# Optimization experiments

Measured on AMD Instinct MI355X. Metric: run time of the kernel, lower is better.

## Reference

```python
import jax, jax.numpy as jnp
import numpy as np

NSAMPLE = 16
LEAKY = 0.1


def _leaky(x):
    return jnp.where(x >= 0, x, LEAKY * x)


def _sqdist(src, dst):
    # src [B,N,3], dst [B,M,3] -> [B,N,M]
    d = -2.0 * jnp.einsum('bnc,bmc->bnm', src, dst)
    d = d + jnp.sum(src * src, -1)[:, :, None]
    d = d + jnp.sum(dst * dst, -1)[:, None, :]
    return d


def _knn_idx(query, points, k):
    # query [B,N,3], points [B,M,3] -> [B,N,k] indices of k nearest points
    dist = _sqdist(query, points)
    _, idx = jax.lax.top_k(-dist, k)
    return idx


def _group(points, idx):
    # points [B,M,C], idx [B,N,K] -> [B,N,K,C]
    return jax.vmap(lambda p, i: p[i])(points, idx)


def _cross(xyz1, xyz2, p1, p2, pos_w, pos_b, mlp_params):
    # xyz1 [B,N1,3], xyz2 [B,N2,3], p1 [B,N1,C], p2 [B,N2,C]
    idx = _knn_idx(xyz1, xyz2, NSAMPLE)                       # [B,N1,K]
    neigh_xyz = _group(xyz2, idx)                             # [B,N1,K,3]
    direction = neigh_xyz - xyz1[:, :, None, :]               # [B,N1,K,3]
    g2 = _group(p2, idx)                                      # [B,N1,K,C]
    pos_feat = jnp.einsum('bnkc,oc->bnko', direction, pos_w) + pos_b
    new_pts = _leaky(g2 + p1[:, :, None, :] + pos_feat)       # [B,N1,K,C0]
    for w, b in mlp_params:
        new_pts = _leaky(jnp.einsum('bnkc,oc->bnko', new_pts, w) + b)
    return jnp.max(new_pts, axis=2)                           # [B,N1,Cl]


def setup_inputs() -> dict:
    key = jax.random.key(0)
    ks = jax.random.split(key, 14)
    B, N, D = 2, 8192, 64
    s = 0.1
    return {
        'pc1': jax.random.normal(ks[0], (B, N, 3), jnp.float32),
        'pc2': jax.random.normal(ks[1], (B, N, 3), jnp.float32),
        'feat1': jax.random.normal(ks[2], (B, N, D), jnp.float32),
        'feat2': jax.random.normal(ks[3], (B, N, D), jnp.float32),
        'pos_w': jax.random.normal(ks[4], (64, 3), jnp.float32) * s,
        'pos_b': jax.random.normal(ks[5], (64,), jnp.float32) * s,
        'mlp_w0': jax.random.normal(ks[6], (64, 64), jnp.float32) * s,
        'mlp_b0': jax.random.normal(ks[7], (64,), jnp.float32) * s,
        'mlp_w1': jax.random.normal(ks[8], (64, 64), jnp.float32) * s,
        'mlp_b1': jax.random.normal(ks[9], (64,), jnp.float32) * s,
        't1_w': jax.random.normal(ks[10], (128, 64), jnp.float32) * s,
        't1_b': jax.random.normal(ks[11], (128,), jnp.float32) * s,
        't2_w': jax.random.normal(ks[12], (128, 64), jnp.float32) * s,
        't2_b': jax.random.normal(ks[13], (128,), jnp.float32) * s,
    }


def reference(pc1, pc2, feat1, feat2, pos_w, pos_b, mlp_w0, mlp_b0,
              mlp_w1, mlp_b1, t1_w, t1_b, t2_w, t2_b):
    mlp = [(mlp_w0, mlp_b0), (mlp_w1, mlp_b1)]
    f1 = _cross(pc1, pc2, feat1, feat2, pos_w, pos_b, mlp)    # [B,N1,64]
    f1 = jnp.einsum('bnc,oc->bno', f1, t1_w) + t1_b           # [B,N1,128]
    f2 = _cross(pc2, pc1, feat2, feat1, pos_w, pos_b, mlp)
    f2 = jnp.einsum('bnc,oc->bno', f2, t2_w) + t2_b
    return f1, f2
```

## Files before the change

kernel.cpp:

```cpp
#include <hip/hip_runtime.h>

#define NPTS 8192
#define KNNK 16
#define NSLOT 17
#define LEAKY 0.1f

typedef short bf16x8 __attribute__((ext_vector_type(8)));
typedef float f32x4  __attribute__((ext_vector_type(4)));

#define KTH   1024
#define QPB   128
#define CHN   32
#define GQ    4
#define BUFCAP 48

__global__ __launch_bounds__(KTH, 4) void knn_kernel(
    const float* __restrict__ pc1, const float* __restrict__ pc2,
    int* __restrict__ knn_out)
{
    __shared__ float sx[NPTS], sy[NPTS], sz[NPTS];
    __shared__ float sbuf[QPB][2 * BUFCAP];
    __shared__ float sthr[QPB];
    __shared__ int   scnt[QPB];

    const int t   = threadIdx.x;
    const int q0  = blockIdx.x * QPB;
    const int dir = q0 >> 14;
    const int b   = (q0 >> 13) & 1;

    const float* __restrict__ pq    = dir ? pc2 : pc1;
    const float* __restrict__ pcand = dir ? pc1 : pc2;

    const float* src = pcand + (size_t)b * NPTS * 3;
    for (int i = t; i < NPTS; i += KTH) {
        sx[i] = src[3 * i];
        sy[i] = src[3 * i + 1];
        sz[i] = src[3 * i + 2];
    }
    if (t < QPB) scnt[t] = 0;
    __syncthreads();

    const int ch = t & (CHN - 1);
    const int qg = t >> 5;
    const int n0 = q0 & (NPTS - 1);

    float q2x[GQ], q2y[GQ], q2z[GQ];
    #pragma unroll
    for (int g = 0; g < GQ; ++g) {
        const float* qp = pq + ((size_t)b * NPTS + n0 + qg * GQ + g) * 3;
        q2x[g] = -2.0f * qp[0];
        q2y[g] = -2.0f * qp[1];
        q2z[g] = -2.0f * qp[2];
    }

    float mA[GQ], mB[GQ];
    #pragma unroll
    for (int g = 0; g < GQ; ++g) { mA[g] = 3.0e38f; mB[g] = 3.0e38f; }

    #pragma unroll 2
    for (int j = 0; j < 32; ++j) {
        const int i0 = j * 128 + 4 * ch;
        const int i1 = i0 + 4096;
        const f32x4 ax = *(const f32x4*)&sx[i0];
        const f32x4 ay = *(const f32x4*)&sy[i0];
        const f32x4 az = *(const f32x4*)&sz[i0];
        const f32x4 bx = *(const f32x4*)&sx[i1];
        const f32x4 by = *(const f32x4*)&sy[i1];
        const f32x4 bz = *(const f32x4*)&sz[i1];
        f32x4 an, bn;
        #pragma unroll
        for (int c = 0; c < 4; ++c) {
            an[c] = fmaf(ax[c], ax[c], fmaf(ay[c], ay[c], az[c] * az[c]));
            bn[c] = fmaf(bx[c], bx[c], fmaf(by[c], by[c], bz[c] * bz[c]));
        }
        #pragma unroll
        for (int g = 0; g < GQ; ++g) {
            #pragma unroll
            for (int c = 0; c < 4; ++c) {
                const float da = fmaf(q2x[g], ax[c],
                                 fmaf(q2y[g], ay[c],
                                 fmaf(q2z[g], az[c], an[c])));
                mA[g] = fminf(mA[g], da);
                const float db = fmaf(q2x[g], bx[c],
                                 fmaf(q2y[g], by[c],
                                 fmaf(q2z[g], bz[c], bn[c])));
                mB[g] = fminf(mB[g], db);
            }
        }
    }

    #pragma unroll
    for (int g = 0; g < GQ; ++g) {
        const int row = qg * GQ + g;
        sbuf[row][ch]      = mA[g];
        sbuf[row][32 + ch] = mB[g];
    }
    __builtin_amdgcn_wave_barrier();

    #pragma unroll
    for (int g = 0; g < GQ; ++g) {
        const int row = qg * GQ + g;
        const float vA = mA[g], vB = mB[g];
        int ltA = 0, eqA = 0, ltB = 0, eqB = 0;
        #pragma unroll
        for (int c = 0; c < 64; c += 2) {
            const float2 vp = *(const float2*)&sbuf[row][c];
            ltA += (vp.x < vA) ? 1 : 0;  eqA += (vp.x == vA) ? 1 : 0;
            ltA += (vp.y < vA) ? 1 : 0;  eqA += (vp.y == vA) ? 1 : 0;
            ltB += (vp.x < vB) ? 1 : 0;  eqB += (vp.x == vB) ? 1 : 0;
            ltB += (vp.y < vB) ? 1 : 0;  eqB += (vp.y == vB) ? 1 : 0;
        }
        if (ltA <= 16 && ltA + eqA > 16) sthr[row] = vA;
        if (ltB <= 16 && ltB + eqB > 16) sthr[row] = vB;
    }
    __builtin_amdgcn_wave_barrier();

    float tq[GQ];
    #pragma unroll
    for (int g = 0; g < GQ; ++g) tq[g] = sthr[qg * GQ + g];

    #pragma unroll 2
    for (int j = 0; j < 64; ++j) {
        const int i0 = j * 128 + 4 * ch;
        const f32x4 cx = *(const f32x4*)&sx[i0];
        const f32x4 cy = *(const f32x4*)&sy[i0];
        const f32x4 cz = *(const f32x4*)&sz[i0];
        f32x4 cn;
        #pragma unroll
        for (int c = 0; c < 4; ++c)
            cn[c] = fmaf(cx[c], cx[c], fmaf(cy[c], cy[c], cz[c] * cz[c]));
        #pragma unroll
        for (int g = 0; g < GQ; ++g) {
            #pragma unroll
            for (int c = 0; c < 4; ++c) {
                const float d = fmaf(q2x[g], cx[c],
                                fmaf(q2y[g], cy[c],
                                fmaf(q2z[g], cz[c], cn[c])));
                if (d <= tq[g]) {
                    const int q = qg * GQ + g;
                    const int pos = atomicAdd(&scnt[q], 1);
                    if (pos < BUFCAP) {
                        sbuf[q][pos] = d;
                        ((int*)&sbuf[q][BUFCAP])[pos] = i0 + c;
                    }
                }
            }
        }
    }
    __syncthreads();

    if (t < QPB) {
        const int nc = min(scnt[t], BUFCAP);

        float dist[NSLOT];
        int   ind[NSLOT];
        #pragma unroll
        for (int i = 0; i < NSLOT; ++i) { dist[i] = 3.0e38f; ind[i] = 0x7fffffff; }

        for (int s = 0; s < nc; ++s) {
            const float d  = sbuf[t][s];
            const int   id = ((int*)&sbuf[t][BUFCAP])[s];
            const bool better0 = (d < dist[0]) || (d == dist[0] && id < ind[0]);
            if (better0) {
                bool cprev = true;
                #pragma unroll
                for (int i = 0; i < NSLOT - 1; ++i) {
                    const bool ci = (d < dist[i + 1]) ||
                                    (d == dist[i + 1] && id < ind[i + 1]);
                    const float nv = ci ? dist[i + 1] : (cprev ? d  : dist[i]);
                    const int   ni = ci ? ind[i + 1]  : (cprev ? id : ind[i]);
                    dist[i] = nv; ind[i] = ni;
                    cprev = ci;
                }
                if (cprev) { dist[NSLOT - 1] = d; ind[NSLOT - 1] = id; }
            }
        }

        const float* qpp = pq + ((size_t)b * NPTS + n0 + t) * 3;
        const double dqx = (double)qpp[0], dqy = (double)qpp[1], dqz = (double)qpp[2];
        double dd[NSLOT];
        #pragma unroll
        for (int i = 0; i < NSLOT; ++i) {
            const int id = ind[i];
            const double dx = (double)sx[id] - dqx;
            const double dy = (double)sy[id] - dqy;
            const double dz = (double)sz[id] - dqz;
            dd[i] = dx * dx + dy * dy + dz * dz;
        }
        int worst = 0; double wd = dd[0];
        #pragma unroll
        for (int i = 1; i < NSLOT; ++i) { if (dd[i] > wd) { wd = dd[i]; worst = i; } }

        int* outp = knn_out + (size_t)(q0 + t) * KNNK;
        int slot = 0;
        #pragma unroll
        for (int i = 0; i < NSLOT; ++i) {
            if (i != worst) outp[slot++] = ind[i];
        }
    }
}

#define PTS 16
#define NG  4

__device__ __forceinline__ unsigned int packhl(float f) {
    const unsigned int u = __float_as_uint(f);
    const unsigned int h = u & 0xffff0000u;
    const float lf = f - __uint_as_float(h);
    return h | (__float_as_uint(lf) >> 16);
}

__device__ __forceinline__ void build_b(const float* __restrict__ wrow,
                                        bf16x8* hi, bf16x8* lo) {
    union { unsigned int u[4]; bf16x8 v; } H, L;
    #pragma unroll
    for (int r = 0; r < 4; ++r) {
        const float f0 = wrow[2 * r], f1 = wrow[2 * r + 1];
        const unsigned int h0 = __float_as_uint(f0) & 0xffff0000u;
        const unsigned int h1 = __float_as_uint(f1) & 0xffff0000u;
        const float l0 = f0 - __uint_as_float(h0);
        const float l1 = f1 - __uint_as_float(h1);
        H.u[r] = h1 | (h0 >> 16);
        L.u[r] = (__float_as_uint(l1) & 0xffff0000u) | (__float_as_uint(l0) >> 16);
    }
    *hi = H.v; *lo = L.v;
}

__device__ __forceinline__ void unpack_a(const unsigned int* __restrict__ Tu,
                                         bf16x8* hi, bf16x8* lo) {
    union { unsigned int u[4]; bf16x8 v; } H, L;
    #pragma unroll
    for (int r = 0; r < 4; ++r) {
        const unsigned int a = Tu[2 * r + 1], bb = Tu[2 * r];
        H.u[r] = __builtin_amdgcn_perm(a, bb, 0x07060302u);
        L.u[r] = __builtin_amdgcn_perm(a, bb, 0x05040100u);
    }
    *hi = H.v; *lo = L.v;
}

__device__ __forceinline__ f32x4 mfma3(f32x4 acc, bf16x8 ah, bf16x8 al,
                                       bf16x8 bh, bf16x8 bl) {
    acc = __builtin_amdgcn_mfma_f32_16x16x32_bf16(ah, bl, acc, 0, 0, 0);
    acc = __builtin_amdgcn_mfma_f32_16x16x32_bf16(al, bh, acc, 0, 0, 0);
    acc = __builtin_amdgcn_mfma_f32_16x16x32_bf16(ah, bh, acc, 0, 0, 0);
    return acc;
}

__global__ __launch_bounds__(256, 4) void feat_kernel(
    const float* __restrict__ pc1, const float* __restrict__ pc2,
    const float* __restrict__ feat1, const float* __restrict__ feat2,
    const float* __restrict__ pos_w, const float* __restrict__ pos_b,
    const float* __restrict__ w0, const float* __restrict__ b0,
    const float* __restrict__ w1, const float* __restrict__ b1,
    const float* __restrict__ t1w, const float* __restrict__ t1b,
    const float* __restrict__ t2w, const float* __restrict__ t2b,
    const int* __restrict__ knn, float* __restrict__ out)
{
    __shared__ unsigned int T0[4][16][68];
    __shared__ unsigned int T1[4][16][68];
    __shared__ float sm[PTS][64];

    const int t    = threadIdx.x;
    const int w    = t >> 6;
    const int lane = t & 63;
    const int m    = lane & 15;
    const int quad = lane >> 4;

    const int p0  = blockIdx.x * PTS;
    const int dir = p0 >> 14, bt = (p0 >> 13) & 1;
    const int n0  = p0 & (NPTS - 1);

    const float* __restrict__ pqd = dir ? pc2 : pc1;
    const float* __restrict__ pcd = dir ? pc1 : pc2;
    const float* __restrict__ fqd = dir ? feat2 : feat1;
    const float* __restrict__ fcd = dir ? feat1 : feat2;

    const int ocol = w * 16 + m;
    bf16x8 Bh[2][2], Bl[2][2];
    #pragma unroll
    for (int kt = 0; kt < 2; ++kt) {
        build_b(&w0[(size_t)ocol * 64 + kt * 32 + quad * 8], &Bh[0][kt], &Bl[0][kt]);
        build_b(&w1[(size_t)ocol * 64 + kt * 32 + quad * 8], &Bh[1][kt], &Bl[1][kt]);
    }
    const float bias1 = b0[ocol];
    const float bias2 = b1[ocol];

    const int cg0 = w * 16 + quad * 4;
    float pbc[4], pwx[4], pwy[4], pwz[4];
    #pragma unroll
    for (int i = 0; i < 4; ++i) {
        pbc[i] = pos_b[cg0 + i];
        pwx[i] = pos_w[(cg0 + i) * 3 + 0];
        pwy[i] = pos_w[(cg0 + i) * 3 + 1];
        pwz[i] = pos_w[(cg0 + i) * 3 + 2];
    }

    float  sdx[4], sdy[4], sdz[4];
    float4 sgf[4], sfq[4];

    auto loadg = [&](int gg) {
        #pragma unroll
        for (int pt = 0; pt < 4; ++pt) {
            const int pp = p0 + gg * 4 + pt;
            const int nn = n0 + gg * 4 + pt;
            const int id = knn[(size_t)pp * KNNK + m];
            const float* qp  = pqd + ((size_t)bt * NPTS + nn) * 3;
            const float* nbp = pcd + ((size_t)bt * NPTS + id) * 3;
            sdx[pt] = nbp[0] - qp[0];
            sdy[pt] = nbp[1] - qp[1];
            sdz[pt] = nbp[2] - qp[2];
            sgf[pt] = *(const float4*)&fcd[((size_t)bt * NPTS + id) * 64 + cg0];
            sfq[pt] = *(const float4*)&fqd[((size_t)bt * NPTS + nn) * 64 + cg0];
        }
    };

    auto storeg = [&]() {
        #pragma unroll
        for (int pt = 0; pt < 4; ++pt) {
            const float gfa[4] = {sgf[pt].x, sgf[pt].y, sgf[pt].z, sgf[pt].w};
            const float fqa[4] = {sfq[pt].x, sfq[pt].y, sfq[pt].z, sfq[pt].w};
            uint4 U;
            unsigned int* Up = (unsigned int*)&U;
            #pragma unroll
            for (int i = 0; i < 4; ++i) {
                float v = gfa[i] + fqa[i] + pbc[i];
                v = fmaf(sdx[pt], pwx[i], v);
                v = fmaf(sdy[pt], pwy[i], v);
                v = fmaf(sdz[pt], pwz[i], v);
                v = fmaxf(v, LEAKY * v);
                Up[i] = packhl(v);
            }
            *(uint4*)&T0[pt][m][cg0] = U;
        }
    };

    loadg(0);
    storeg();
    __syncthreads();

    #pragma unroll
    for (int g = 0; g < NG; ++g) {
        if (g + 1 < NG) loadg(g + 1);

        #pragma unroll
        for (int pt = 0; pt < 4; ++pt) {
            unsigned int Tu[8];
            bf16x8 Ah, Al;
            f32x4 acc = {0.f, 0.f, 0.f, 0.f};
            #pragma unroll
            for (int kt = 0; kt < 2; ++kt) {
                *(uint4*)&Tu[0] = *(const uint4*)&T0[pt][m][kt * 32 + quad * 8];
                *(uint4*)&Tu[4] = *(const uint4*)&T0[pt][m][kt * 32 + quad * 8 + 4];
                unpack_a(Tu, &Ah, &Al);
                acc = mfma3(acc, Ah, Al, Bh[0][kt], Bl[0][kt]);
            }
            #pragma unroll
            for (int r = 0; r < 4; ++r) {
                float v = acc[r] + bias1;
                v = fmaxf(v, LEAKY * v);
                T1[pt][quad * 4 + r][ocol] = packhl(v);
            }
        }
        __syncthreads();

        if (g + 1 < NG) storeg();

        #pragma unroll
        for (int pt = 0; pt < 4; ++pt) {
            unsigned int Tu[8];
            bf16x8 Ah, Al;
            f32x4 acc = {0.f, 0.f, 0.f, 0.f};
            #pragma unroll
            for (int kt = 0; kt < 2; ++kt) {
                *(uint4*)&Tu[0] = *(const uint4*)&T1[pt][m][kt * 32 + quad * 8];
                *(uint4*)&Tu[4] = *(const uint4*)&T1[pt][m][kt * 32 + quad * 8 + 4];
                unpack_a(Tu, &Ah, &Al);
                acc = mfma3(acc, Ah, Al, Bh[1][kt], Bl[1][kt]);
            }
            float mx = -3.0e38f;
            #pragma unroll
            for (int r = 0; r < 4; ++r) {
                float v = acc[r] + bias2;
                v = fmaxf(v, LEAKY * v);
                mx = fmaxf(mx, v);
            }
            mx = fmaxf(mx, __shfl_xor(mx, 16));
            mx = fmaxf(mx, __shfl_xor(mx, 32));
            if (quad == 0) sm[g * 4 + pt][ocol] = mx;
        }
        __syncthreads();
    }

    {
        const float* __restrict__ tw = dir ? t2w : t1w;
        const float* __restrict__ tb = dir ? t2b : t1b;
        const int o  = t & 127;
        const int pg = t >> 7;
        float acc[8];
        const float bz = tb[o];
        #pragma unroll
        for (int i = 0; i < 8; ++i) acc[i] = bz;
        #pragma unroll
        for (int cc = 0; cc < 64; cc += 4) {
            const float4 wq = *(const float4*)&tw[(size_t)o * 64 + cc];
            #pragma unroll
            for (int pr = 0; pr < 4; ++pr) {
                const int pa = (2 * pr + pg) * 2;
                const float4 a0 = *(const float4*)&sm[pa][cc];
                const float4 a1 = *(const float4*)&sm[pa + 1][cc];
                float x0 = acc[2 * pr], x1 = acc[2 * pr + 1];
                x0 = fmaf(a0.x, wq.x, x0); x0 = fmaf(a0.y, wq.y, x0);
                x0 = fmaf(a0.z, wq.z, x0); x0 = fmaf(a0.w, wq.w, x0);
                x1 = fmaf(a1.x, wq.x, x1); x1 = fmaf(a1.y, wq.y, x1);
                x1 = fmaf(a1.z, wq.z, x1); x1 = fmaf(a1.w, wq.w, x1);
                acc[2 * pr] = x0; acc[2 * pr + 1] = x1;
            }
        }
        float* op = out + (size_t)dir * (2 * NPTS * 128);
        #pragma unroll
        for (int pr = 0; pr < 4; ++pr) {
            const int pa = (2 * pr + pg) * 2;
            op[((size_t)bt * NPTS + n0 + pa) * 128 + o]     = acc[2 * pr];
            op[((size_t)bt * NPTS + n0 + pa + 1) * 128 + o] = acc[2 * pr + 1];
        }
    }
}

extern "C" void kernel_launch(void* const* d_in, const int* in_sizes, int n_in,
                              void* d_out, int out_size, void* d_ws, size_t ws_size,
                              hipStream_t stream)
{
    const float* pc1   = (const float*)d_in[0];
    const float* pc2   = (const float*)d_in[1];
    const float* feat1 = (const float*)d_in[2];
    const float* feat2 = (const float*)d_in[3];
    const float* pos_w = (const float*)d_in[4];
    const float* pos_b = (const float*)d_in[5];
    const float* w0    = (const float*)d_in[6];
    const float* b0    = (const float*)d_in[7];
    const float* w1    = (const float*)d_in[8];
    const float* b1    = (const float*)d_in[9];
    const float* t1w   = (const float*)d_in[10];
    const float* t1b   = (const float*)d_in[11];
    const float* t2w   = (const float*)d_in[12];
    const float* t2b   = (const float*)d_in[13];

    int*   knn = (int*)d_ws;
    float* out = (float*)d_out;

    hipLaunchKernelGGL(knn_kernel, dim3(32768 / QPB), dim3(KTH), 0, stream,
                       pc1, pc2, knn);
    hipLaunchKernelGGL(feat_kernel, dim3(32768 / PTS), dim3(256), 0, stream,
                       pc1, pc2, feat1, feat2, pos_w, pos_b,
                       w0, b0, w1, b1, t1w, t1b, t2w, t2b, knn, out);
}
```

Baseline: 265.0 us.

## Rescan only candidate chunks whose minimum beats the threshold via shared work list

Instead of rescanning all 8192 candidates per query in the second KNN pass, each thread's per-chunk minima from the first pass are compared to the query's threshold, and only chunks that can contain a neighbor are pushed to a shared work list. All threads of the block then split the listed chunks into sub-work items and recompute distances only for those. This removes most of the redundant second-pass distance work, at the cost of extra shared memory (a list and query coefficients), atomics on a shared counter, a block-wide barrier, and a silent cap on list size that could drop candidates if exceeded.

Result: faster. 256.5 us (-3.2%).

```diff
diff --git a/kernel.cpp b/kernel.cpp
--- a/kernel.cpp
+++ b/kernel.cpp
@@ -13,6 +13,7 @@
 #define CHN   32
 #define GQ    4
 #define BUFCAP 48
+#define LCAP  6144
 
 __global__ __launch_bounds__(KTH, 4) void knn_kernel(
     const float* __restrict__ pc1, const float* __restrict__ pc2,
@@ -22,6 +23,9 @@
     __shared__ float sbuf[QPB][2 * BUFCAP];
     __shared__ float sthr[QPB];
     __shared__ int   scnt[QPB];
+    __shared__ float4 qcoef[QPB];
+    __shared__ unsigned short list[LCAP];
+    __shared__ int   lcnt;
 
     const int t   = threadIdx.x;
     const int q0  = blockIdx.x * QPB;
@@ -30,6 +34,7 @@
 
     const float* __restrict__ pq    = dir ? pc2 : pc1;
     const float* __restrict__ pcand = dir ? pc1 : pc2;
+    const int n0 = q0 & (NPTS - 1);
 
     const float* src = pcand + (size_t)b * NPTS * 3;
     for (int i = t; i < NPTS; i += KTH) {
@@ -37,12 +42,16 @@
         sy[i] = src[3 * i + 1];
         sz[i] = src[3 * i + 2];
     }
-    if (t < QPB) scnt[t] = 0;
+    if (t < QPB) {
+        scnt[t] = 0;
+        const float* qp = pq + ((size_t)b * NPTS + n0 + t) * 3;
+        qcoef[t] = make_float4(-2.0f * qp[0], -2.0f * qp[1], -2.0f * qp[2], 0.f);
+    }
+    if (t == 0) lcnt = 0;
     __syncthreads();
 
     const int ch = t & (CHN - 1);
     const int qg = t >> 5;
-    const int n0 = q0 & (NPTS - 1);
 
     float q2x[GQ], q2y[GQ], q2z[GQ];
     #pragma unroll
@@ -113,35 +122,52 @@
         if (ltA <= 16 && ltA + eqA > 16) sthr[row] = vA;
         if (ltB <= 16 && ltB + eqB > 16) sthr[row] = vB;
     }
-    __builtin_amdgcn_wave_barrier();
-
-    float tq[GQ];
-    #pragma unroll
-    for (int g = 0; g < GQ; ++g) tq[g] = sthr[qg * GQ + g];
-
-    #pragma unroll 2
-    for (int j = 0; j < 64; ++j) {
-        const int i0 = j * 128 + 4 * ch;
-        const f32x4 cx = *(const f32x4*)&sx[i0];
-        const f32x4 cy = *(const f32x4*)&sy[i0];
-        const f32x4 cz = *(const f32x4*)&sz[i0];
-        f32x4 cn;
-        #pragma unroll
-        for (int c = 0; c < 4; ++c)
-            cn[c] = fmaf(cx[c], cx[c], fmaf(cy[c], cy[c], cz[c] * cz[c]));
-        #pragma unroll
-        for (int g = 0; g < GQ; ++g) {
-            #pragma unroll
-            for (int c = 0; c < 4; ++c) {
-                const float d = fmaf(q2x[g], cx[c],
-                                fmaf(q2y[g], cy[c],
-                                fmaf(q2z[g], cz[c], cn[c])));
-                if (d <= tq[g]) {
-                    const int q = qg * GQ + g;
-                    const int pos = atomicAdd(&scnt[q], 1);
-                    if (pos < BUFCAP) {
-                        sbuf[q][pos] = d;
-                        ((int*)&sbuf[q][BUFCAP])[pos] = i0 + c;
+    __syncthreads();
+
+    #pragma unroll
+    for (int g = 0; g < GQ; ++g) {
+        const int row = qg * GQ + g;
+        const float tqv = sthr[row];
+        if (mA[g] <= tqv) {
+            const int p = atomicAdd(&lcnt, 1);
+            if (p < LCAP) list[p] = (unsigned short)((row << 6) | ch);
+        }
+        if (mB[g] <= tqv) {
+            const int p = atomicAdd(&lcnt, 1);
+            if (p < LCAP) list[p] = (unsigned short)((row << 6) | 32 | ch);
+        }
+    }
+    __syncthreads();
+
+    {
+        const int nsub = min(lcnt, LCAP) * 8;
+        for (int k = t; k < nsub; k += KTH) {
+            const int e  = list[k >> 3];
+            const int s  = k & 7;
+            const int q  = e >> 6;
+            const int hf = (e >> 5) & 1;
+            const int cc = e & 31;
+            const float4 qc = qcoef[q];
+            const float tqv = sthr[q];
+            #pragma unroll
+            for (int jj = 0; jj < 4; ++jj) {
+                const int i0 = hf * 4096 + (s * 4 + jj) * 128 + 4 * cc;
+                const f32x4 cx = *(const f32x4*)&sx[i0];
+                const f32x4 cy = *(const f32x4*)&sy[i0];
+                const f32x4 cz = *(const f32x4*)&sz[i0];
+                #pragma unroll
+                for (int c = 0; c < 4; ++c) {
+                    const float cn = fmaf(cx[c], cx[c],
+                                     fmaf(cy[c], cy[c], cz[c] * cz[c]));
+                    const float d  = fmaf(qc.x, cx[c],
+                                     fmaf(qc.y, cy[c],
+                                     fmaf(qc.z, cz[c], cn)));
+                    if (d <= tqv) {
+                        const int pos = atomicAdd(&scnt[q], 1);
+                        if (pos < BUFCAP) {
+                            sbuf[q][pos] = d;
+                            ((int*)&sbuf[q][BUFCAP])[pos] = i0 + c;
+                        }
                     }
                 }
             }
```
